# Kernel tuning notes

Hardware: AMD Instinct MI355X
Metric: run time of the kernel (lower is better)

## Reference

```python
import jax, jax.numpy as jnp
import numpy as np

D_MODEL = 768
MIMO_RANK = 4


def setup_inputs() -> dict:
    key = jax.random.key(0)
    ks = jax.random.split(key, 6)
    B, T, D, R = 2, 2048, D_MODEL, MIMO_RANK
    x = jax.random.normal(ks[0], (B, T, D), dtype=jnp.float32)
    norm_w = jnp.ones((D,), dtype=jnp.float32)
    W_in = jax.random.normal(ks[1], (D * R * 2, D), dtype=jnp.float32) * 0.02
    W_out = jax.random.normal(ks[2], (D, D), dtype=jnp.float32) * 0.02
    a_param = jax.random.normal(ks[3], (D, R, 2), dtype=jnp.float32) * 0.12
    b_param = jax.random.normal(ks[4], (D, R, 2), dtype=jnp.float32) * 0.15
    c_param = jax.random.normal(ks[5], (D, R, 2), dtype=jnp.float32) * 0.15
    return {"x": x, "norm_w": norm_w, "W_in": W_in, "W_out": W_out,
            "a_param": a_param, "b_param": b_param, "c_param": c_param}


def reference(x, norm_w, W_in, W_out, a_param, b_param, c_param):
    B, T, D = x.shape
    R = a_param.shape[1]
    # RMSNorm
    xn = x * jax.lax.rsqrt(jnp.mean(x * x, axis=-1, keepdims=True) + 1e-6) * norm_w
    # in_proj -> interleaved complex MIMO input u: [B,T,D,R,2]
    u = (xn @ W_in.T).reshape(B, T, D, R, 2)
    # coefficients (tanh-bounded; |a| scaled by 0.97 for stability)
    a = jnp.tanh(a_param) * 0.97
    b = jnp.tanh(b_param)
    c = jnp.tanh(c_param)
    ac = jax.lax.complex(a[..., 0], a[..., 1])  # [D,R]
    bc = jax.lax.complex(b[..., 0], b[..., 1])
    cc = jax.lax.complex(c[..., 0], c[..., 1])
    uc = jax.lax.complex(u[..., 0], u[..., 1])  # [B,T,D,R]
    # linear complex recurrence s_t = a * s_{t-1} + b * u_t, zero init state,
    # parallelized with an associative scan over time.
    bu = bc[None, None] * uc
    A = jnp.broadcast_to(ac[None, None], bu.shape)

    def comb(l, r):
        return (l[0] * r[0], r[0] * l[1] + r[1])

    _, s = jax.lax.associative_scan(comb, (A, bu), axis=1)  # [B,T,D,R] complex
    # output mix: real part of c * h, summed over MIMO rank -> [B,T,D]
    y = jnp.real(cc[None, None] * s).sum(axis=-1)
    return y @ W_out.T
```

## Files before the change

kernel.cpp:

```cpp
#include <hip/hip_runtime.h>
#include <hip/hip_bf16.h>
#include <stdint.h>

#define BATCH 2
#define TT 2048
#define DM 768
#define RR 4
#define M_TOK 4096
#define NFEAT 6144
#define NCH 6144
#define CHUNK 64
#define NCHUNK 32

typedef __attribute__((ext_vector_type(8))) short short8;
typedef __attribute__((ext_vector_type(4))) float float4v;

__device__ inline float bf2f(uint32_t bits16) {
    union { uint32_t u; float f; } x; x.u = bits16 << 16; return x.f;
}

typedef const __attribute__((address_space(1))) void* gptr_t;
typedef __attribute__((address_space(3))) void* lptr_t;

__device__ inline void async_ld16(const void* g, void* l) {
    __builtin_amdgcn_global_load_lds((gptr_t)(uintptr_t)g, (lptr_t)(uintptr_t)l,
                                     16, 0, 0);
}

__device__ inline void store_c(__hip_bfloat16* C, size_t idx, float v) {
    C[idx] = __float2bfloat16(v);
}
__device__ inline void store_c(float* C, size_t idx, float v) { C[idx] = v; }

__device__ inline uint2 pack4bf(float a, float b, float c, float d) {
    union { __hip_bfloat16 h[4]; uint2 u; } o;
    o.h[0] = __float2bfloat16(a); o.h[1] = __float2bfloat16(b);
    o.h[2] = __float2bfloat16(c); o.h[3] = __float2bfloat16(d);
    return o.u;
}

__device__ inline uint32_t pack2bf(float a, float b) {
    union { __hip_bfloat16 h[2]; uint32_t u; } o;
    o.h[0] = __float2bfloat16(a); o.h[1] = __float2bfloat16(b);
    return o.u;
}

__device__ inline float2 cmul(float2 a, float2 b) {
    return make_float2(a.x * b.x - a.y * b.y, a.x * b.y + a.y * b.x);
}

__device__ inline void cstep(float& sr, float& si, float2 a, float2 bb,
                             uint32_t uw) {
    float ur = bf2f(uw & 0xffffu), ui = bf2f(uw >> 16);
    float tr = bb.x * ur - bb.y * ui;
    float ti = bb.x * ui + bb.y * ur;
    float nr = a.x * sr - a.y * si + tr;
    float ni = a.x * si + a.y * sr + ti;
    sr = nr; si = ni;
}

__global__ __launch_bounds__(256) void prep_rms(
    const float* __restrict__ x, const float* __restrict__ w,
    const float* __restrict__ W_in, const float* __restrict__ W_out,
    const float* __restrict__ ap, const float* __restrict__ bp,
    const float* __restrict__ cp,
    __hip_bfloat16* __restrict__ xn,
    __hip_bfloat16* __restrict__ Win_bf, __hip_bfloat16* __restrict__ Wout_bf,
    float2* __restrict__ ac, float2* __restrict__ bc,
    float2* __restrict__ cc, float2* __restrict__ aL) {
    int bid = blockIdx.x;
    int tid = threadIdx.x;
    if (bid < M_TOK) {
        __shared__ float wsum[3];
        float4 v = make_float4(0.f, 0.f, 0.f, 0.f);
        if (tid < 192) v = ((const float4*)(x + (size_t)bid * DM))[tid];
        float ss = v.x * v.x + v.y * v.y + v.z * v.z + v.w * v.w;
        #pragma unroll
        for (int o = 1; o < 64; o <<= 1) ss += __shfl_xor(ss, o);
        if (tid < 192 && (tid & 63) == 0) wsum[tid >> 6] = ss;
        __syncthreads();
        if (tid < 192) {
            float tot = wsum[0] + wsum[1] + wsum[2];
            float scale = rsqrtf(tot * (1.f / DM) + 1e-6f);
            float4 wv = ((const float4*)w)[tid];
            ((uint2*)(xn + (size_t)bid * DM))[tid] =
                pack4bf(v.x * scale * wv.x, v.y * scale * wv.y,
                        v.z * scale * wv.z, v.w * scale * wv.w);
        }
        return;
    }
    const int N1 = NFEAT * DM / 4;
    const int N2 = DM * DM / 4;
    int i = (bid - M_TOK) * 256 + tid;
    if (i < N1) {
        float4 v = ((const float4*)W_in)[i];
        ((uint2*)Win_bf)[i] = pack4bf(v.x, v.y, v.z, v.w);
    } else if (i < N1 + N2) {
        int k = i - N1;
        float4 v = ((const float4*)W_out)[k];
        ((uint2*)Wout_bf)[k] = pack4bf(v.x, v.y, v.z, v.w);
    }
    if (i < DM * RR) {
        float ar = tanhf(ap[2 * i])     * 0.97f;
        float ai = tanhf(ap[2 * i + 1]) * 0.97f;
        ac[i] = make_float2(ar, ai);
        bc[i] = make_float2(tanhf(bp[2 * i]), tanhf(bp[2 * i + 1]));
        cc[i] = make_float2(tanhf(cp[2 * i]), tanhf(cp[2 * i + 1]));
        float xr = ar, xi = ai;
        #pragma unroll
        for (int k = 0; k < 6; ++k) {
            float nr = xr * xr - xi * xi;
            float ni = 2.f * xr * xi;
            xr = nr; xi = ni;
        }
        aL[i] = make_float2(xr, xi);
    }
}

template <int BM, int BN, int BK, typename OutT>
__device__ inline void gemm_body(
    const __hip_bfloat16* __restrict__ A, const __hip_bfloat16* __restrict__ B,
    OutT* __restrict__ C, int K, int ldc) {
    constexpr int MI = BM / 32;
    constexpr int NJ = BN / 32;
    constexpr int CPR = BK / 8;
    __shared__ __attribute__((aligned(16))) __hip_bfloat16 lA[BM * BK];
    __shared__ __attribute__((aligned(16))) __hip_bfloat16 lB[BN * BK];
    const int tid  = threadIdx.x;
    const int lane = tid & 63;
    const int wave = tid >> 6;
    const int quad = lane >> 4;
    const int l15  = lane & 15;
    const int wm = (wave >> 1) * (BM / 2);
    const int wn = (wave & 1) * (BN / 2);
    const int m0 = blockIdx.y * BM;
    const int n0 = blockIdx.x * BN;

    float4v acc[MI][NJ] = {};

    for (int k0 = 0; k0 < K; k0 += BK) {
        __syncthreads();
        #pragma unroll
        for (int it = 0; it < BM * CPR / 256; ++it) {
            int p = it * 256 + tid;
            int row = p / CPR;
            int cg = (p & (CPR - 1)) ^ (row & (CPR - 1));
            async_ld16(A + (size_t)(m0 + row) * K + k0 + cg * 8, lA + p * 8);
        }
        #pragma unroll
        for (int it = 0; it < BN * CPR / 256; ++it) {
            int p = it * 256 + tid;
            int row = p / CPR;
            int cg = (p & (CPR - 1)) ^ (row & (CPR - 1));
            async_ld16(B + (size_t)(n0 + row) * K + k0 + cg * 8, lB + p * 8);
        }
        __syncthreads();
        #pragma unroll
        for (int s = 0; s < BK / 32; ++s) {
            short8 af[MI], bfr[NJ];
            #pragma unroll
            for (int i = 0; i < MI; ++i) {
                int r = wm + i * 16 + l15;
                int c = (s * 4 + quad) ^ (r & (CPR - 1));
                af[i] = *(const short8*)(lA + r * BK + c * 8);
            }
            #pragma unroll
            for (int j = 0; j < NJ; ++j) {
                int r = wn + j * 16 + l15;
                int c = (s * 4 + quad) ^ (r & (CPR - 1));
                bfr[j] = *(const short8*)(lB + r * BK + c * 8);
            }
            #pragma unroll
            for (int i = 0; i < MI; ++i)
                #pragma unroll
                for (int j = 0; j < NJ; ++j)
                    acc[i][j] = __builtin_amdgcn_mfma_f32_16x16x32_bf16(
                        af[i], bfr[j], acc[i][j], 0, 0, 0);
        }
    }
    #pragma unroll
    for (int i = 0; i < MI; ++i)
        #pragma unroll
        for (int j = 0; j < NJ; ++j)
            #pragma unroll
            for (int rg = 0; rg < 4; ++rg) {
                int row = m0 + wm + i * 16 + quad * 4 + rg;
                int col = n0 + wn + j * 16 + l15;
                store_c(C, (size_t)row * ldc + col, acc[i][j][rg]);
            }
}

__global__ __launch_bounds__(256) void gemm_out(
    const __hip_bfloat16* __restrict__ A, const __hip_bfloat16* __restrict__ B,
    float* __restrict__ C, int K) {
    gemm_body<64, 64, 128, float>(A, B, C, K, DM);
}

__global__ __launch_bounds__(256) void gemm_in_scan(
    const __hip_bfloat16* __restrict__ A,
    const __hip_bfloat16* __restrict__ B,
    const float2* __restrict__ ac, const float2* __restrict__ bc,
    const float2* __restrict__ cc,
    __hip_bfloat16* __restrict__ y_local,
    float2* __restrict__ chunkEnd) {
    constexpr int BM = 128, BN = 128, BK = 64;
    constexpr int MI = BM / 32, NJ = BN / 32, CPR = BK / 8;
    constexpr int K = DM;
    __shared__ __attribute__((aligned(16))) __hip_bfloat16 smem[BM * BK + BN * BK];
    __hip_bfloat16* lA = smem;
    __hip_bfloat16* lB = smem + BM * BK;
    const int tid  = threadIdx.x;
    const int lane = tid & 63;
    const int wave = tid >> 6;
    const int quad = lane >> 4;
    const int l15  = lane & 15;
    const int wm = (wave >> 1) * (BM / 2);
    const int wn = (wave & 1) * (BN / 2);
    const int m0 = blockIdx.y * BM;
    const int n0 = blockIdx.x * BN;

    float4v acc[MI][NJ] = {};

    for (int k0 = 0; k0 < K; k0 += BK) {
        __syncthreads();
        #pragma unroll
        for (int it = 0; it < BM * CPR / 256; ++it) {
            int p = it * 256 + tid;
            int row = p / CPR;
            int cg = (p & (CPR - 1)) ^ (row & (CPR - 1));
            async_ld16(A + (size_t)(m0 + row) * K + k0 + cg * 8, lA + p * 8);
        }
        #pragma unroll
        for (int it = 0; it < BN * CPR / 256; ++it) {
            int p = it * 256 + tid;
            int row = p / CPR;
            int cg = (p & (CPR - 1)) ^ (row & (CPR - 1));
            async_ld16(B + (size_t)(n0 + row) * K + k0 + cg * 8, lB + p * 8);
        }
        __syncthreads();
        #pragma unroll
        for (int s = 0; s < BK / 32; ++s) {
            short8 af[MI], bfr[NJ];
            #pragma unroll
            for (int i = 0; i < MI; ++i) {
                int r = wm + i * 16 + l15;
                int c = (s * 4 + quad) ^ (r & (CPR - 1));
                af[i] = *(const short8*)(lA + r * BK + c * 8);
            }
            #pragma unroll
            for (int j = 0; j < NJ; ++j) {
                int r = wn + j * 16 + l15;
                int c = (s * 4 + quad) ^ (r & (CPR - 1));
                bfr[j] = *(const short8*)(lB + r * BK + c * 8);
            }
            #pragma unroll
            for (int i = 0; i < MI; ++i)
                #pragma unroll
                for (int j = 0; j < NJ; ++j)
                    acc[i][j] = __builtin_amdgcn_mfma_f32_16x16x32_bf16(
                        af[i], bfr[j], acc[i][j], 0, 0, 0);
        }
    }

    __syncthreads();
    uint32_t* up = (uint32_t*)smem;
    #pragma unroll
    for (int i = 0; i < MI; ++i)
        #pragma unroll
        for (int j = 0; j < NJ; ++j) {
            float s0 = __shfl_xor(acc[i][j][0], 1);
            float s1 = __shfl_xor(acc[i][j][1], 1);
            float s2 = __shfl_xor(acc[i][j][2], 1);
            float s3 = __shfl_xor(acc[i][j][3], 1);
            const bool odd = l15 & 1;
            float lo0 = odd ? s2 : acc[i][j][0];
            float hi0 = odd ? acc[i][j][2] : s0;
            float lo1 = odd ? s3 : acc[i][j][1];
            float hi1 = odd ? acc[i][j][3] : s1;
            int row0 = wm + i * 16 + quad * 4 + (odd ? 2 : 0);
            int row1 = row0 + 1;
            int pr = (wn + j * 16 + (l15 & ~1)) >> 1;
            up[row0 * 64 + (pr ^ (row0 & 31))] = pack2bf(lo0, hi0);
            up[row1 * 64 + (pr ^ (row1 & 31))] = pack2bf(lo1, hi1);
        }
    __syncthreads();

    if (tid < 128) {
        const int r     = tid & 3;
        const int d_loc = (tid >> 2) & 15;
        const int half  = tid >> 6;
        const int d_g   = (n0 >> 3) + d_loc;
        const int cb    = d_g * RR + r;
        const float2 av = ac[cb];
        const float2 bv = bc[cb];
        const float2 cv = cc[cb];
        const int bb = m0 >> 11;
        const int j  = ((m0 & (TT - 1)) >> 6) + half;
        const int p  = d_loc * 4 + r;
        float sr = 0.f, si = 0.f;
        size_t ybase = (size_t)(m0 + half * 64) * DM + d_g;
        #pragma unroll 4
        for (int t = 0; t < CHUNK; ++t) {
            int row = half * 64 + t;
            uint32_t uw = up[row * 64 + (p ^ (row & 31))];
            cstep(sr, si, av, bv, uw);
            float yv = cv.x * sr - cv.y * si;
            yv += __shfl_xor(yv, 1);
            yv += __shfl_xor(yv, 2);
            if (r == 0)
                y_local[ybase + (size_t)t * DM] = __float2bfloat16(yv);
        }
        chunkEnd[(size_t)j * NCH + bb * (DM * RR) + cb] = make_float2(sr, si);
    }
}

__global__ __launch_bounds__(256) void scan_fix(
    const __hip_bfloat16* __restrict__ y_local,
    const float2* __restrict__ ac, const float2* __restrict__ cc,
    const float2* __restrict__ aLp, const float2* __restrict__ chunkEnd,
    __hip_bfloat16* __restrict__ y) {
    int g = blockIdx.x * 256 + threadIdx.x;
    int j = blockIdx.y;
    int b = g >= DM;
    int d = g - b * DM;
    int cb = d * RR;
    float2 a0 = ac[cb], a1 = ac[cb + 1], a2 = ac[cb + 2], a3 = ac[cb + 3];
    float2 aL0 = aLp[cb], aL1 = aLp[cb + 1], aL2 = aLp[cb + 2], aL3 = aLp[cb + 3];
    float2 k0 = make_float2(0, 0), k1 = k0, k2 = k0, k3 = k0;
    for (int jj = 0; jj < j; ++jj) {
        size_t eb = (size_t)jj * NCH + b * (DM * RR) + cb;
        float2 e0 = chunkEnd[eb],     e1 = chunkEnd[eb + 1];
        float2 e2 = chunkEnd[eb + 2], e3 = chunkEnd[eb + 3];
        float nr, ni;
        nr = aL0.x * k0.x - aL0.y * k0.y + e0.x; ni = aL0.x * k0.y + aL0.y * k0.x + e0.y; k0 = make_float2(nr, ni);
        nr = aL1.x * k1.x - aL1.y * k1.y + e1.x; ni = aL1.x * k1.y + aL1.y * k1.x + e1.y; k1 = make_float2(nr, ni);
        nr = aL2.x * k2.x - aL2.y * k2.y + e2.x; ni = aL2.x * k2.y + aL2.y * k2.x + e2.y; k2 = make_float2(nr, ni);
        nr = aL3.x * k3.x - aL3.y * k3.y + e3.x; ni = aL3.x * k3.y + aL3.y * k3.x + e3.y; k3 = make_float2(nr, ni);
    }
    float2 q0 = cmul(cmul(cc[cb],     k0), a0);
    float2 q1 = cmul(cmul(cc[cb + 1], k1), a1);
    float2 q2 = cmul(cmul(cc[cb + 2], k2), a2);
    float2 q3 = cmul(cmul(cc[cb + 3], k3), a3);
    size_t base = ((size_t)(b * TT + j * CHUNK)) * DM + d;
    #pragma unroll 4
    for (int i = 0; i < CHUNK; ++i) {
        float yv = bf2f(((const uint16_t*)y_local)[base + (size_t)i * DM])
                 + q0.x + q1.x + q2.x + q3.x;
        y[base + (size_t)i * DM] = __float2bfloat16(yv);
        q0 = cmul(q0, a0); q1 = cmul(q1, a1);
        q2 = cmul(q2, a2); q3 = cmul(q3, a3);
    }
}

extern "C" void kernel_launch(void* const* d_in, const int* in_sizes, int n_in,
                              void* d_out, int out_size, void* d_ws,
                              size_t ws_size, hipStream_t stream) {
    const float* x      = (const float*)d_in[0];
    const float* norm_w = (const float*)d_in[1];
    const float* W_in   = (const float*)d_in[2];
    const float* W_out  = (const float*)d_in[3];
    const float* a_p    = (const float*)d_in[4];
    const float* b_p    = (const float*)d_in[5];
    const float* c_p    = (const float*)d_in[6];
    float* out = (float*)d_out;

    char* ws = (char*)d_ws;
    size_t off = 0;
    auto alloc = [&](size_t bytes) {
        void* p = ws + off;
        off += (bytes + 255) & ~(size_t)255;
        return p;
    };
    __hip_bfloat16* Win_bf  = (__hip_bfloat16*)alloc((size_t)NFEAT * DM * 2);
    __hip_bfloat16* Wout_bf = (__hip_bfloat16*)alloc((size_t)DM * DM * 2);
    __hip_bfloat16* xn      = (__hip_bfloat16*)alloc((size_t)M_TOK * DM * 2);
    __hip_bfloat16* y_local = (__hip_bfloat16*)alloc((size_t)M_TOK * DM * 2);
    __hip_bfloat16* y       = (__hip_bfloat16*)alloc((size_t)M_TOK * DM * 2);
    float2* ac = (float2*)alloc((size_t)DM * RR * 8);
    float2* bc = (float2*)alloc((size_t)DM * RR * 8);
    float2* cc = (float2*)alloc((size_t)DM * RR * 8);
    float2* aL = (float2*)alloc((size_t)DM * RR * 8);
    float2* chunkEnd = (float2*)alloc((size_t)NCHUNK * NCH * 8);

    {
        int cast_blocks = ((NFEAT * DM + DM * DM) / 4 + 255) / 256;
        prep_rms<<<M_TOK + cast_blocks, 256, 0, stream>>>(
            x, norm_w, W_in, W_out, a_p, b_p, c_p,
            xn, Win_bf, Wout_bf, ac, bc, cc, aL);
    }
    gemm_in_scan<<<dim3(NFEAT / 128, M_TOK / 128), 256, 0, stream>>>(
        xn, Win_bf, ac, bc, cc, y_local, chunkEnd);
    scan_fix<<<dim3(BATCH * DM / 256, NCHUNK), 256, 0, stream>>>(
        y_local, ac, cc, aL, chunkEnd, y);
    gemm_out<<<dim3(DM / 64, M_TOK / 64), 256, 0, stream>>>(
        y, Wout_bf, out, DM);
}
```

Before: 199.5 us.

## Scan all four ranks per thread in fused epilogue and split fixup over sub-chunks

In the GEMM epilogue, each scan thread now handles all four MIMO ranks of one channel. It reads a 16-byte vector from LDS under a new swizzle, which removes the cross-lane shuffles and the rank-0-only global store, but only 32 threads now run the serial scan instead of 128. The scan_fix kernel gains a third grid dimension that splits each 64-step chunk into four 16-step pieces. Each piece fast-forwards its carry with a precomputed a^16 power (aQ), which adds parallelism to the fixup pass at the cost of redundant prefix recomputation across the pieces.

```diff
diff --git a/kernel.cpp b/kernel.cpp
--- a/kernel.cpp
+++ b/kernel.cpp
@@ -67,7 +67,8 @@
     __hip_bfloat16* __restrict__ xn,
     __hip_bfloat16* __restrict__ Win_bf, __hip_bfloat16* __restrict__ Wout_bf,
     float2* __restrict__ ac, float2* __restrict__ bc,
-    float2* __restrict__ cc, float2* __restrict__ aL) {
+    float2* __restrict__ cc, float2* __restrict__ aQ,
+    float2* __restrict__ aL) {
     int bid = blockIdx.x;
     int tid = threadIdx.x;
     if (bid < M_TOK) {
@@ -108,7 +109,14 @@
         cc[i] = make_float2(tanhf(cp[2 * i]), tanhf(cp[2 * i + 1]));
         float xr = ar, xi = ai;
         #pragma unroll
-        for (int k = 0; k < 6; ++k) {
+        for (int k = 0; k < 4; ++k) {
+            float nr = xr * xr - xi * xi;
+            float ni = 2.f * xr * xi;
+            xr = nr; xi = ni;
+        }
+        aQ[i] = make_float2(xr, xi);
+        #pragma unroll
+        for (int k = 0; k < 2; ++k) {
             float nr = xr * xr - xi * xi;
             float ni = 2.f * xr * xi;
             xr = nr; xi = ni;
@@ -280,47 +288,57 @@
             int row0 = wm + i * 16 + quad * 4 + (odd ? 2 : 0);
             int row1 = row0 + 1;
             int pr = (wn + j * 16 + (l15 & ~1)) >> 1;
-            up[row0 * 64 + (pr ^ (row0 & 31))] = pack2bf(lo0, hi0);
-            up[row1 * 64 + (pr ^ (row1 & 31))] = pack2bf(lo1, hi1);
+            int sl = pr & 3;
+            up[row0 * 64 + (((pr >> 2) ^ (row0 & 15)) << 2) + sl] =
+                pack2bf(lo0, hi0);
+            up[row1 * 64 + (((pr >> 2) ^ (row1 & 15)) << 2) + sl] =
+                pack2bf(lo1, hi1);
         }
     __syncthreads();
 
-    if (tid < 128) {
-        const int r     = tid & 3;
-        const int d_loc = (tid >> 2) & 15;
-        const int half  = tid >> 6;
+    if (tid < 32) {
+        const int d_loc = tid & 15;
+        const int half  = tid >> 4;
         const int d_g   = (n0 >> 3) + d_loc;
-        const int cb    = d_g * RR + r;
-        const float2 av = ac[cb];
-        const float2 bv = bc[cb];
-        const float2 cv = cc[cb];
+        const int cb    = d_g * RR;
+        float2 a0 = ac[cb], a1 = ac[cb + 1], a2 = ac[cb + 2], a3 = ac[cb + 3];
+        float2 b0 = bc[cb], b1 = bc[cb + 1], b2 = bc[cb + 2], b3 = bc[cb + 3];
+        float2 c0 = cc[cb], c1 = cc[cb + 1], c2 = cc[cb + 2], c3 = cc[cb + 3];
         const int bb = m0 >> 11;
         const int j  = ((m0 & (TT - 1)) >> 6) + half;
-        const int p  = d_loc * 4 + r;
-        float sr = 0.f, si = 0.f;
+        const uint4* up4 = (const uint4*)smem;
+        float s0r = 0, s0i = 0, s1r = 0, s1i = 0;
+        float s2r = 0, s2i = 0, s3r = 0, s3i = 0;
         size_t ybase = (size_t)(m0 + half * 64) * DM + d_g;
         #pragma unroll 4
         for (int t = 0; t < CHUNK; ++t) {
             int row = half * 64 + t;
-            uint32_t uw = up[row * 64 + (p ^ (row & 31))];
-            cstep(sr, si, av, bv, uw);
-            float yv = cv.x * sr - cv.y * si;
-            yv += __shfl_xor(yv, 1);
-            yv += __shfl_xor(yv, 2);
-            if (r == 0)
-                y_local[ybase + (size_t)t * DM] = __float2bfloat16(yv);
-        }
-        chunkEnd[(size_t)j * NCH + bb * (DM * RR) + cb] = make_float2(sr, si);
+            uint4 uw = up4[row * 16 + (d_loc ^ (row & 15))];
+            cstep(s0r, s0i, a0, b0, uw.x);
+            cstep(s1r, s1i, a1, b1, uw.y);
+            cstep(s2r, s2i, a2, b2, uw.z);
+            cstep(s3r, s3i, a3, b3, uw.w);
+            float yv = c0.x * s0r - c0.y * s0i + c1.x * s1r - c1.y * s1i
+                     + c2.x * s2r - c2.y * s2i + c3.x * s3r - c3.y * s3i;
+            y_local[ybase + (size_t)t * DM] = __float2bfloat16(yv);
+        }
+        size_t eb = (size_t)j * NCH + bb * (DM * RR) + cb;
+        chunkEnd[eb]     = make_float2(s0r, s0i);
+        chunkEnd[eb + 1] = make_float2(s1r, s1i);
+        chunkEnd[eb + 2] = make_float2(s2r, s2i);
+        chunkEnd[eb + 3] = make_float2(s3r, s3i);
     }
 }
 
 __global__ __launch_bounds__(256) void scan_fix(
     const __hip_bfloat16* __restrict__ y_local,
     const float2* __restrict__ ac, const float2* __restrict__ cc,
-    const float2* __restrict__ aLp, const float2* __restrict__ chunkEnd,
+    const float2* __restrict__ aQp, const float2* __restrict__ aLp,
+    const float2* __restrict__ chunkEnd,
     __hip_bfloat16* __restrict__ y) {
     int g = blockIdx.x * 256 + threadIdx.x;
     int j = blockIdx.y;
+    int z = blockIdx.z;
     int b = g >= DM;
     int d = g - b * DM;
     int cb = d * RR;
@@ -341,9 +359,14 @@
     float2 q1 = cmul(cmul(cc[cb + 1], k1), a1);
     float2 q2 = cmul(cmul(cc[cb + 2], k2), a2);
     float2 q3 = cmul(cmul(cc[cb + 3], k3), a3);
-    size_t base = ((size_t)(b * TT + j * CHUNK)) * DM + d;
+    float2 aQ0 = aQp[cb], aQ1 = aQp[cb + 1], aQ2 = aQp[cb + 2], aQ3 = aQp[cb + 3];
+    for (int zz = 0; zz < z; ++zz) {
+        q0 = cmul(q0, aQ0); q1 = cmul(q1, aQ1);
+        q2 = cmul(q2, aQ2); q3 = cmul(q3, aQ3);
+    }
+    size_t base = ((size_t)(b * TT + j * CHUNK + z * 16)) * DM + d;
     #pragma unroll 4
-    for (int i = 0; i < CHUNK; ++i) {
+    for (int i = 0; i < 16; ++i) {
         float yv = bf2f(((const uint16_t*)y_local)[base + (size_t)i * DM])
                  + q0.x + q1.x + q2.x + q3.x;
         y[base + (size_t)i * DM] = __float2bfloat16(yv);
@@ -379,6 +402,7 @@
     float2* ac = (float2*)alloc((size_t)DM * RR * 8);
     float2* bc = (float2*)alloc((size_t)DM * RR * 8);
     float2* cc = (float2*)alloc((size_t)DM * RR * 8);
+    float2* aQ = (float2*)alloc((size_t)DM * RR * 8);
     float2* aL = (float2*)alloc((size_t)DM * RR * 8);
     float2* chunkEnd = (float2*)alloc((size_t)NCHUNK * NCH * 8);
 
@@ -386,12 +410,12 @@
         int cast_blocks = ((NFEAT * DM + DM * DM) / 4 + 255) / 256;
         prep_rms<<<M_TOK + cast_blocks, 256, 0, stream>>>(
             x, norm_w, W_in, W_out, a_p, b_p, c_p,
-            xn, Win_bf, Wout_bf, ac, bc, cc, aL);
+            xn, Win_bf, Wout_bf, ac, bc, cc, aQ, aL);
     }
     gemm_in_scan<<<dim3(NFEAT / 128, M_TOK / 128), 256, 0, stream>>>(
         xn, Win_bf, ac, bc, cc, y_local, chunkEnd);
-    scan_fix<<<dim3(BATCH * DM / 256, NCHUNK), 256, 0, stream>>>(
-        y_local, ac, cc, aL, chunkEnd, y);
+    scan_fix<<<dim3(BATCH * DM / 256, NCHUNK, 4), 256, 0, stream>>>(
+        y_local, ac, cc, aQ, aL, chunkEnd, y);
     gemm_out<<<dim3(DM / 64, M_TOK / 64), 256, 0, stream>>>(
         y, Wout_bf, out, DM);
 }
```

New measurement: 198.7 us. No clear change (-0.4%).
